# Kernel optimization log

Measured on AMD Instinct MI355X. Metric: run time of the kernel, lower is better.

## Reference

```python
import jax, jax.numpy as jnp
import numpy as np

B, C, H, W = 16, 2, 768, 768
WIN = 5                      # window_size: maxima kernel AND gauss-fit window
PAD = WIN // 2
HEATMAP_AXIS = 1
THRESHOLD = 0.5
MAX_DET = 393216             # fixed-size pad for data-dependent nonzero()


def setup_inputs() -> dict:
    key = jax.random.key(0)
    # strictly positive heat so log(z) in Guo's fit is well-defined
    x = jax.random.uniform(key, (B, C, H, W), dtype=jnp.float32, minval=1e-4, maxval=1.0)
    return {"x": x}


def _forward(x):
    heat = x[:, HEATMAP_AXIS]                                   # [B,H,W]
    th = jnp.where(heat > THRESHOLD, heat, 0.0)
    # kornia dilation with ones kernel (center zeroed) == max over neighbors excl. center
    padded = jnp.pad(th, ((0, 0), (PAD, PAD), (PAD, PAD)), constant_values=-np.inf)
    dilated = jnp.full(th.shape, -np.inf, th.dtype)
    for dy in range(WIN):
        for dx in range(WIN):
            if dy == PAD and dx == PAD:
                continue
            dilated = jnp.maximum(dilated, padded[:, dy:dy + H, dx:dx + W])
    local_max = (th > dilated).reshape(-1)                      # strict local maxima above threshold
    (flat_idx,) = jnp.nonzero(local_max, size=MAX_DET, fill_value=0)  # row-major, like torch.nonzero
    valid = jnp.arange(MAX_DET) < local_max.sum()
    bidx = flat_idx // (H * W)
    rc = flat_idx % (H * W)
    r = rc // W
    cc = rc % W
    sub = jnp.linspace((-WIN) // 2 + 1, WIN // 2, WIN)
    xs, ys = jnp.meshgrid(sub, sub, indexing='xy')              # xs varies along columns
    xf = xs.reshape(-1).astype(jnp.float32)                     # [K]
    yf = ys.reshape(-1).astype(jnp.float32)
    off = jnp.arange(WIN) - PAD
    off_r = jnp.repeat(off, WIN)                                # row-major window flattening
    off_c = jnp.tile(off, WIN)
    rows = jnp.clip(r[:, None] + off_r[None, :], 0, H - 1)      # clamp at borders
    cols = jnp.clip(cc[:, None] + off_c[None, :], 0, W - 1)
    z = heat[bidx[:, None], rows, cols]                         # [N,K] window intensities
    z = jnp.clip(z, 1e-6, None)                                 # numerical guard for log
    xb = jnp.broadcast_to(xf, z.shape)
    yb = jnp.broadcast_to(yf, z.shape)
    # quadratic basis [1, x, x^2, y, xy, y^2]
    basis = jnp.stack([jnp.ones_like(xb), xb, xb * xb, yb, xb * yb, yb * yb], -1)  # [N,K,6]
    wgt = z * z                                                  # Guo's weights
    Aw = basis * wgt[:, :, None]
    bvec = jnp.log(z) * wgt
    ATA = jnp.einsum('nki,nkj->nij', Aw, Aw)                     # [N,6,6]
    ATb = jnp.einsum('nki,nk->ni', Aw, bvec)                     # [N,6]
    coef = jnp.einsum('nij,nj->ni', jnp.linalg.inv(ATA), ATb)    # [N,6]
    Aq, Bl, Cc = coef[:, [2, 5]], coef[:, [1, 3]], coef[:, [0, 4]]
    good = valid & jnp.all(Aq < 0, axis=-1)                      # concave fit -> real sigma
    g = good[:, None]
    Aq_s = jnp.where(g, Aq, -0.5)                                # guard against NaN at padded slots
    sigma = jnp.sqrt(-1.0 / (2.0 * Aq_s))
    mu = Bl * sigma ** 2
    height = jnp.exp(jnp.where(g, Cc + 0.5 * mu ** 2 / sigma ** 2, 0.0))
    pos = jnp.stack([r, cc], -1).astype(jnp.float32) + mu[:, ::-1]  # maxima_indices + mu[:,[1,0]]
    sigma = jnp.where(g, sigma, 0.0)
    pos = jnp.where(g, pos, 0.0)
    height = jnp.where(g, height, 0.0)
    return sigma, pos, height, good


def reference(x):
    return _forward(x)
```

## Files before the change

### kernel.cpp

```cpp
#include <hip/hip_runtime.h>
#include <hip/hip_bf16.h>
#include <cstdint>

#define BATCH 16
#define HDIM 768
#define WDIM 768
#define HW (HDIM * WDIM)
#define NPIX (BATCH * HW)
#define MAX_DET 393216
#define NWORDS (NPIX / 64)
#define SCAT_BLOCKS 576
#define WPB 256

#define MASK_OFF 0u
#define CNT_OFF  1179648u
#define TOT_OFF  1187840u
#define IDX_OFF  1188096u

#define SIGMA_BASE 0
#define POS_BASE   786432
#define HGT_BASE   1572864
#define GOOD_BASE  2359296

#define TILE_C 256
#define TILE_R 32
#define LDS_C 264
#define LDS_R 36
#define VEC_PER_ROW 66
#define TOT_VEC (LDS_R * VEC_PER_ROW)

__device__ __forceinline__ double fast_log_f32(float zf) {
    int ib = __float_as_int(zf);
    int e = ((ib >> 23) & 255) - 127;
    float m1 = __int_as_float((ib & 0x007fffff) | 0x3f800000);
    float lg = __builtin_amdgcn_logf(m1);
    return ((double)e + (double)lg) * 0.6931471805599453;
}

__device__ __forceinline__ double fast_rcp(double d) {
    double r = (double)__builtin_amdgcn_rcpf((float)d);
    r = r * (2.0 - d * r);
    r = r * (2.0 - d * r);
    return r;
}

__global__ __launch_bounds__(256) void mask_kernel(const float* __restrict__ x,
                                                   unsigned long long* __restrict__ mask) {
    __shared__ float lds[LDS_R * LDS_C];
    const int bid = blockIdx.x;
    const int b   = bid / 72;
    const int rem = bid - b * 72;
    const int rt  = rem / 3;
    const int cs  = rem - rt * 3;
    const int r0  = rt * TILE_R;
    const int tid = threadIdx.x;
    const float* heat = x + (size_t)b * (2 * HW) + HW;

    const int colbase = cs * TILE_C - 4;
    #pragma unroll
    for (int i = 0; i < 10; ++i) {
        int idx = i * 256 + tid;
        if (idx < TOT_VEC) {
            int lr = (unsigned)idx / VEC_PER_ROW;
            int q  = idx - lr * VEC_PER_ROW;
            int row = r0 - 2 + lr;
            int col = colbase + 4 * q;
            float4 v = make_float4(0.f, 0.f, 0.f, 0.f);
            if (row >= 0 && row < HDIM && col >= 0 && col <= WDIM - 4) {
                v = *reinterpret_cast<const float4*>(heat + (size_t)row * WDIM + col);
            }
            float4 t;
            t.x = v.x > 0.5f ? v.x : 0.f;
            t.y = v.y > 0.5f ? v.y : 0.f;
            t.z = v.z > 0.5f ? v.z : 0.f;
            t.w = v.w > 0.5f ? v.w : 0.f;
            *reinterpret_cast<float4*>(&lds[lr * LDS_C + 4 * q]) = t;
        }
    }
    __syncthreads();

    const int wv   = tid >> 6;
    const int lane = tid & 63;
    const int lrow0 = wv * 8;

    auto readrow = [&](int ldsrow, float* h5, float* hx, float* tc) {
        const float* p = &lds[ldsrow * LDS_C + 4 * lane];
        float4 a = *reinterpret_cast<const float4*>(p);
        float4 bb = *reinterpret_cast<const float4*>(p + 4);
        float4 cc = *reinterpret_cast<const float4*>(p + 8);
        float t2=a.z,t3=a.w,t4=bb.x,t5=bb.y,t6=bb.z,t7=bb.w,t8=cc.x,t9=cc.y;
        float pp0=fmaxf(t2,t3), pp1=fmaxf(t3,t4), pp2=fmaxf(t4,t5), pp3=fmaxf(t5,t6),
              pp4=fmaxf(t6,t7), pp5=fmaxf(t7,t8), pp6=fmaxf(t8,t9);
        h5[0]=fmaxf(fmaxf(pp0,pp2),t6);  hx[0]=fmaxf(pp0,pp3);  tc[0]=t4;
        h5[1]=fmaxf(fmaxf(pp1,pp3),t7);  hx[1]=fmaxf(pp1,pp4);  tc[1]=t5;
        h5[2]=fmaxf(fmaxf(pp2,pp4),t8);  hx[2]=fmaxf(pp2,pp5);  tc[2]=t6;
        h5[3]=fmaxf(fmaxf(pp3,pp5),t9);  hx[3]=fmaxf(pp3,pp6);  tc[3]=t7;
    };

    float h5r[5][4], hxr[5][4], tcr[5][4];
    #pragma unroll
    for (int j = 0; j < 4; ++j)
        readrow(lrow0 + j, h5r[j], hxr[j], tcr[j]);

    const int wordbase = b * (HW / 64) + (r0 + wv * 8) * 12 + cs * 4;

    #pragma unroll
    for (int k = 0; k < 8; ++k) {
        readrow(lrow0 + k + 4, h5r[(k+4)%5], hxr[(k+4)%5], tcr[(k+4)%5]);
        unsigned nib = 0;
        #pragma unroll
        for (int c = 0; c < 4; ++c) {
            float dil = fmaxf(fmaxf(h5r[k%5][c], h5r[(k+1)%5][c]),
                        fmaxf(hxr[(k+2)%5][c],
                        fmaxf(h5r[(k+3)%5][c], h5r[(k+4)%5][c])));
            if (tcr[(k+2)%5][c] > dil) nib |= (1u << c);
        }
        unsigned long long w = (unsigned long long)nib << ((lane & 15) * 4);
        w |= __shfl_xor(w, 1);
        w |= __shfl_xor(w, 2);
        w |= __shfl_xor(w, 4);
        w |= __shfl_xor(w, 8);
        if ((lane & 15) == 0) mask[wordbase + k * 12 + (lane >> 4)] = w;
    }
}

__global__ __launch_bounds__(WPB) void count_kernel(const unsigned long long* __restrict__ mask,
                                                    int* __restrict__ counts) {
    __shared__ int s[WPB];
    int t = threadIdx.x;
    int w = blockIdx.x * WPB + t;
    s[t] = __popcll(mask[w]);
    __syncthreads();
    for (int off = WPB / 2; off > 0; off >>= 1) {
        if (t < off) s[t] += s[t + off];
        __syncthreads();
    }
    if (t == 0) counts[blockIdx.x] = s[0];
}

__global__ __launch_bounds__(WPB) void scatter_kernel(const unsigned long long* __restrict__ mask,
                                                      const int* __restrict__ counts,
                                                      int* __restrict__ flat_idx,
                                                      int* __restrict__ total) {
    __shared__ int s[WPB];
    __shared__ int blockoff;
    const int t = threadIdx.x;
    const int bid = blockIdx.x;

    int acc = 0;
    for (int i = t; i < bid; i += WPB) acc += counts[i];
    s[t] = acc;
    __syncthreads();
    for (int off = WPB / 2; off > 0; off >>= 1) {
        if (t < off) s[t] += s[t + off];
        __syncthreads();
    }
    if (t == 0) blockoff = s[0];
    __syncthreads();

    if (bid == 0) {
        int a2 = 0;
        for (int i = t; i < SCAT_BLOCKS; i += WPB) a2 += counts[i];
        s[t] = a2;
        __syncthreads();
        for (int off = WPB / 2; off > 0; off >>= 1) {
            if (t < off) s[t] += s[t + off];
            __syncthreads();
        }
        if (t == 0) *total = s[0];
        __syncthreads();
    }

    int w = bid * WPB + t;
    unsigned long long m = mask[w];
    int cnt = __popcll(m);
    s[t] = cnt;
    __syncthreads();
    for (int off = 1; off < WPB; off <<= 1) {
        int add = (t >= off) ? s[t - off] : 0;
        __syncthreads();
        s[t] += add;
        __syncthreads();
    }
    int base = blockoff + s[t] - cnt;
    int idx0 = w << 6;
    while (m) {
        int j = __builtin_ctzll(m);
        if (base < MAX_DET) flat_idx[base] = idx0 + j;
        ++base;
        m &= m - 1;
    }
}

__global__ __launch_bounds__(256) void fit_kernel(const float* __restrict__ x,
                                                  const int* __restrict__ flat_idx,
                                                  const int* __restrict__ total,
                                                  float* __restrict__ out) {
    int n = blockIdx.x * 256 + threadIdx.x;
    int count = *total;
    float sx = 0.f, sy = 0.f, p0 = 0.f, p1 = 0.f, h0 = 0.f, h1 = 0.f, goodf = 0.f;
    if (n < count) {
        int idx = flat_idx[n];
        int b = idx / HW;
        int rc = idx - b * HW;
        int r = rc / WDIM;
        int c = rc - r * WDIM;
        const float* heat = x + (size_t)b * (2 * HW) + HW;

        double M00=0,M10=0,M01=0,M20=0,M11=0,M02=0,M30=0,M21=0,M12=0,M03=0;
        double M40=0,M31=0,M22=0,M13=0,M04=0;
        double N0=0,N1=0,N2=0,N3=0,N4=0,N5=0;
        #pragma unroll
        for (int dy = -2; dy <= 2; ++dy) {
            int rr = min(max(r + dy, 0), HDIM - 1);
            const float* hp = heat + (size_t)rr * WDIM;
            double S0=0,S1=0,S2=0,S3=0,S4=0,T0=0,T1=0,T2=0;
            #pragma unroll
            for (int dx = -2; dx <= 2; ++dx) {
                int cc = min(max(c + dx, 0), WDIM - 1);
                float zf = fmaxf(hp[cc], 1e-6f);
                double z = (double)zf;
                double z2 = z * z;
                double w2 = z2 * z2;
                double wl = w2 * fast_log_f32(zf);
                const double X = (double)dx;
                S0 += w2; T0 += wl;
                if (dx != 0) {
                    S1 += w2 * X;
                    S2 += w2 * (X * X);
                    S3 += w2 * (X * X * X);
                    S4 += w2 * (X * X * X * X);
                    T1 += wl * X;
                    T2 += wl * (X * X);
                }
            }
            const double Y = (double)dy;
            M00 += S0; M10 += S1; M20 += S2; M30 += S3; M40 += S4;
            N0 += T0; N1 += T1; N2 += T2;
            if (dy != 0) {
                double Y2 = Y * Y, Y3 = Y2 * Y, Y4 = Y2 * Y2;
                M01 += S0 * Y;  M11 += S1 * Y;  M21 += S2 * Y;  M31 += S3 * Y;
                M02 += S0 * Y2; M12 += S1 * Y2; M22 += S2 * Y2;
                M03 += S0 * Y3; M13 += S1 * Y3;
                M04 += S0 * Y4;
                N3 += T0 * Y; N4 += T1 * Y; N5 += T0 * Y2;
            }
        }

        double A[6][7];
        A[0][0]=M00; A[0][1]=M10; A[0][2]=M20; A[0][3]=M01; A[0][4]=M11; A[0][5]=M02; A[0][6]=N0;
        A[1][0]=M10; A[1][1]=M20; A[1][2]=M30; A[1][3]=M11; A[1][4]=M21; A[1][5]=M12; A[1][6]=N1;
        A[2][0]=M20; A[2][1]=M30; A[2][2]=M40; A[2][3]=M21; A[2][4]=M31; A[2][5]=M22; A[2][6]=N2;
        A[3][0]=M01; A[3][1]=M11; A[3][2]=M21; A[3][3]=M02; A[3][4]=M12; A[3][5]=M03; A[3][6]=N3;
        A[4][0]=M11; A[4][1]=M21; A[4][2]=M31; A[4][3]=M12; A[4][4]=M22; A[4][5]=M13; A[4][6]=N4;
        A[5][0]=M02; A[5][1]=M12; A[5][2]=M22; A[5][3]=M03; A[5][4]=M13; A[5][5]=M04; A[5][6]=N5;

        #pragma unroll
        for (int i = 0; i < 6; ++i) {
            double inv = fast_rcp(A[i][i]);
            #pragma unroll
            for (int j = i + 1; j < 7; ++j) A[i][j] *= inv;
            #pragma unroll
            for (int ii = i + 1; ii < 6; ++ii) {
                double f = A[ii][i];
                #pragma unroll
                for (int j = i + 1; j < 7; ++j) A[ii][j] -= f * A[i][j];
            }
        }
        double cv[6];
        #pragma unroll
        for (int i = 5; i >= 0; --i) {
            double v = A[i][6];
            #pragma unroll
            for (int j = i + 1; j < 6; ++j) v -= A[i][j] * cv[j];
            cv[i] = v;
        }

        double aqx = cv[2], aqy = cv[5];
        if (aqx < 0.0 && aqy < 0.0) {
            double sx2 = -0.5 * fast_rcp(aqx);
            double sy2 = -0.5 * fast_rcp(aqy);
            sx2 = fmin(sx2, 1e300);
            sy2 = fmin(sy2, 1e300);
            double sigx = sqrt(sx2), sigy = sqrt(sy2);
            double mux = cv[1] * sx2, muy = cv[3] * sy2;
            sx = (float)sigx;
            sy = (float)sigy;
            p0 = (float)((double)r + muy);
            p1 = (float)((double)c + mux);
            float a0 = (float)((cv[0] + 0.5 * cv[1] * cv[1] * sx2) * 1.4426950408889634);
            float a1 = (float)((cv[4] + 0.5 * cv[3] * cv[3] * sy2) * 1.4426950408889634);
            a0 = fminf(a0, 126.0f);
            a1 = fminf(a1, 126.0f);
            h0 = exp2f(a0);
            h1 = exp2f(a1);
            goodf = 1.0f;
        }
    }
    out[SIGMA_BASE + 2 * n]     = sx;
    out[SIGMA_BASE + 2 * n + 1] = sy;
    out[POS_BASE + 2 * n]       = p0;
    out[POS_BASE + 2 * n + 1]   = p1;
    out[HGT_BASE + 2 * n]       = h0;
    out[HGT_BASE + 2 * n + 1]   = h1;
    out[GOOD_BASE + n]          = goodf;
}

extern "C" void kernel_launch(void* const* d_in, const int* in_sizes, int n_in,
                              void* d_out, int out_size, void* d_ws, size_t ws_size,
                              hipStream_t stream) {
    const float* x = (const float*)d_in[0];
    float* out = (float*)d_out;
    char* ws = (char*)d_ws;

    unsigned long long* mask = (unsigned long long*)(ws + MASK_OFF);
    int* counts  = (int*)(ws + CNT_OFF);
    int* total   = (int*)(ws + TOT_OFF);
    int* flatidx = (int*)(ws + IDX_OFF);

    mask_kernel<<<BATCH * 24 * 3, 256, 0, stream>>>(x, mask);
    count_kernel<<<SCAT_BLOCKS, WPB, 0, stream>>>(mask, counts);
    scatter_kernel<<<SCAT_BLOCKS, WPB, 0, stream>>>(mask, counts, flatidx, total);
    fit_kernel<<<MAX_DET / 256, 256, 0, stream>>>(x, flatidx, total, out);
}
```

Before: 48.96 us.

## Accumulate fit moments in fp32 and pack mask words through LDS

The fit kernel now computes the window moment sums and the log in single precision instead of double, which cuts the cost of FP64 arithmetic in the per-detection moment accumulation. The mask kernel stops doing a shuffle reduction per row and instead packs 4-bit nibbles per thread into one word. That word goes through LDS, and 128 threads then assemble and store the 64-bit mask words. The fp32 accumulation risks lower accuracy in the later 6x6 solve, and the LDS repack adds two barriers.

Measured after the change: 45.83 us, median of 2. 1.07x faster.

```diff
diff --git a/kernel.cpp b/kernel.cpp
--- a/kernel.cpp
+++ b/kernel.cpp
@@ -29,12 +29,12 @@
 #define VEC_PER_ROW 66
 #define TOT_VEC (LDS_R * VEC_PER_ROW)
 
-__device__ __forceinline__ double fast_log_f32(float zf) {
+__device__ __forceinline__ float fast_logf(float zf) {
     int ib = __float_as_int(zf);
     int e = ((ib >> 23) & 255) - 127;
     float m1 = __int_as_float((ib & 0x007fffff) | 0x3f800000);
     float lg = __builtin_amdgcn_logf(m1);
-    return ((double)e + (double)lg) * 0.6931471805599453;
+    return ((float)e + lg) * 0.69314718055994531f;
 }
 
 __device__ __forceinline__ double fast_rcp(double d) {
@@ -102,8 +102,7 @@
     for (int j = 0; j < 4; ++j)
         readrow(lrow0 + j, h5r[j], hxr[j], tcr[j]);
 
-    const int wordbase = b * (HW / 64) + (r0 + wv * 8) * 12 + cs * 4;
-
+    unsigned nibword = 0;
     #pragma unroll
     for (int k = 0; k < 8; ++k) {
         readrow(lrow0 + k + 4, h5r[(k+4)%5], hxr[(k+4)%5], tcr[(k+4)%5]);
@@ -115,12 +114,32 @@
                         fmaxf(h5r[(k+3)%5][c], h5r[(k+4)%5][c])));
             if (tcr[(k+2)%5][c] > dil) nib |= (1u << c);
         }
-        unsigned long long w = (unsigned long long)nib << ((lane & 15) * 4);
-        w |= __shfl_xor(w, 1);
-        w |= __shfl_xor(w, 2);
-        w |= __shfl_xor(w, 4);
-        w |= __shfl_xor(w, 8);
-        if ((lane & 15) == 0) mask[wordbase + k * 12 + (lane >> 4)] = w;
+        nibword |= nib << (4 * k);
+    }
+
+    __syncthreads();
+    unsigned* lu = (unsigned*)lds;
+    lu[tid] = nibword;
+    __syncthreads();
+    if (tid < 128) {
+        const int wv2 = tid >> 5;
+        const int k2  = (tid >> 2) & 7;
+        const int wi  = tid & 3;
+        const int s   = 4 * k2;
+        const uint4* p = (const uint4*)&lu[wv2 * 64 + wi * 16];
+        uint4 q0 = p[0], q1 = p[1], q2 = p[2], q3 = p[3];
+        unsigned lo = 0, hi = 0;
+        lo |= ((q0.x >> s) & 0xFu) << 0;   lo |= ((q0.y >> s) & 0xFu) << 4;
+        lo |= ((q0.z >> s) & 0xFu) << 8;   lo |= ((q0.w >> s) & 0xFu) << 12;
+        lo |= ((q1.x >> s) & 0xFu) << 16;  lo |= ((q1.y >> s) & 0xFu) << 20;
+        lo |= ((q1.z >> s) & 0xFu) << 24;  lo |= ((q1.w >> s) & 0xFu) << 28;
+        hi |= ((q2.x >> s) & 0xFu) << 0;   hi |= ((q2.y >> s) & 0xFu) << 4;
+        hi |= ((q2.z >> s) & 0xFu) << 8;   hi |= ((q2.w >> s) & 0xFu) << 12;
+        hi |= ((q3.x >> s) & 0xFu) << 16;  hi |= ((q3.y >> s) & 0xFu) << 20;
+        hi |= ((q3.z >> s) & 0xFu) << 24;  hi |= ((q3.w >> s) & 0xFu) << 28;
+        unsigned long long word = (unsigned long long)lo |
+                                  ((unsigned long long)hi << 32);
+        mask[b * (HW / 64) + (r0 + wv2 * 8 + k2) * 12 + cs * 4 + wi] = word;
     }
 }
 
@@ -207,23 +226,22 @@
         int c = rc - r * WDIM;
         const float* heat = x + (size_t)b * (2 * HW) + HW;
 
-        double M00=0,M10=0,M01=0,M20=0,M11=0,M02=0,M30=0,M21=0,M12=0,M03=0;
-        double M40=0,M31=0,M22=0,M13=0,M04=0;
-        double N0=0,N1=0,N2=0,N3=0,N4=0,N5=0;
+        float M00=0,M10=0,M01=0,M20=0,M11=0,M02=0,M30=0,M21=0,M12=0,M03=0;
+        float M40=0,M31=0,M22=0,M13=0,M04=0;
+        float N0=0,N1=0,N2=0,N3=0,N4=0,N5=0;
         #pragma unroll
         for (int dy = -2; dy <= 2; ++dy) {
             int rr = min(max(r + dy, 0), HDIM - 1);
             const float* hp = heat + (size_t)rr * WDIM;
-            double S0=0,S1=0,S2=0,S3=0,S4=0,T0=0,T1=0,T2=0;
+            float S0=0,S1=0,S2=0,S3=0,S4=0,T0=0,T1=0,T2=0;
             #pragma unroll
             for (int dx = -2; dx <= 2; ++dx) {
                 int cc = min(max(c + dx, 0), WDIM - 1);
                 float zf = fmaxf(hp[cc], 1e-6f);
-                double z = (double)zf;
-                double z2 = z * z;
-                double w2 = z2 * z2;
-                double wl = w2 * fast_log_f32(zf);
-                const double X = (double)dx;
+                float z2 = zf * zf;
+                float w2 = z2 * z2;
+                float wl = w2 * fast_logf(zf);
+                const float X = (float)dx;
                 S0 += w2; T0 += wl;
                 if (dx != 0) {
                     S1 += w2 * X;
@@ -234,11 +252,11 @@
                     T2 += wl * (X * X);
                 }
             }
-            const double Y = (double)dy;
+            const float Y = (float)dy;
             M00 += S0; M10 += S1; M20 += S2; M30 += S3; M40 += S4;
             N0 += T0; N1 += T1; N2 += T2;
             if (dy != 0) {
-                double Y2 = Y * Y, Y3 = Y2 * Y, Y4 = Y2 * Y2;
+                float Y2 = Y * Y, Y3 = Y2 * Y, Y4 = Y2 * Y2;
                 M01 += S0 * Y;  M11 += S1 * Y;  M21 += S2 * Y;  M31 += S3 * Y;
                 M02 += S0 * Y2; M12 += S1 * Y2; M22 += S2 * Y2;
                 M03 += S0 * Y3; M13 += S1 * Y3;
```
